# Kernel tuning notes

Measured on AMD Instinct MI355X. Metric: run time of the kernel, lower is better.

The kernel has to match this reference:

```python
import jax, jax.numpy as jnp
import numpy as np

N = 100000   # node_num
D = 256      # enforce_dim
L = 3        # num_layer
E = 200000   # interactions in update batch
B = 50000    # query pairs
W_DECAY = 1e-06
P = 2 * L + 2          # stacked projections per pair
F = P * P              # pair_wise_feature_dim = 64


def setup_inputs() -> dict:
    key = jax.random.key(0)
    ks = jax.random.split(key, 12)
    std = 1.0 / np.sqrt(D)
    inp = {}
    # random projection tables (layer 0 is the random base; layers 1..L are accumulated state)
    inp['rp0'] = jax.random.normal(ks[0], (N, D), jnp.float32) * std
    inp['rp1'] = jax.random.normal(ks[1], (N, D), jnp.float32) * std
    inp['rp2'] = jax.random.normal(ks[2], (N, D), jnp.float32) * std
    inp['rp3'] = jax.random.normal(ks[3], (N, D), jnp.float32) * std
    # sorted interaction timestamps in [0, 1e6]; next_time = times[-1]
    inp['times'] = jnp.sort(jax.random.uniform(ks[4], (E,), jnp.float32) * 1e6)
    inp['now_time'] = jnp.zeros((1,), jnp.float32)
    # MLP: 64 -> 256 -> 64 (stored as [in, out])
    inp['w1'] = jax.random.normal(ks[5], (F, 4 * F), jnp.float32) * (1.0 / np.sqrt(F))
    inp['b1'] = jnp.zeros((4 * F,), jnp.float32)
    inp['w2'] = jax.random.normal(ks[6], (4 * F, F), jnp.float32) * (1.0 / np.sqrt(4 * F))
    inp['b2'] = jnp.zeros((F,), jnp.float32)
    inp['src_ids'] = jax.random.randint(ks[7], (E,), 0, N, jnp.int32)
    inp['dst_ids'] = jax.random.randint(ks[8], (E,), 0, N, jnp.int32)
    inp['q_src'] = jax.random.randint(ks[9], (B,), 0, N, jnp.int32)
    inp['q_dst'] = jax.random.randint(ks[10], (B,), 0, N, jnp.int32)
    return inp


def _update_and_pairwise(rp0, rp1, rp2, rp3, times, now_time, w1, b1, w2, b2,
                         src_ids, dst_ids, q_src, q_dst):
    next_time = times[-1]
    decay = jnp.exp(-W_DECAY * (next_time - now_time[0]))
    # decay accumulated tables: rp[i] *= decay**i for i >= 1
    rps = [rp0, rp1 * decay, rp2 * decay ** 2, rp3 * decay ** 3]
    tw = jnp.exp(-W_DECAY * (next_time - times))[:, None]   # [E,1]
    # update(): for each layer i (all using the pre-update rp[i-1]):
    #   rp[i][src] += rp[i-1][dst] * tw ; rp[i][dst] += rp[i-1][src] * tw
    new = [rps[0]]
    for i in range(1, L + 1):
        upd = rps[i].at[src_ids].add(rps[i - 1][dst_ids] * tw)
        upd = upd.at[dst_ids].add(rps[i - 1][src_ids] * tw)
        new.append(upd)
    # get_pair_wise_feature()
    src_proj = jnp.stack([r[q_src] for r in new], axis=1)   # [B, L+1, D]
    dst_proj = jnp.stack([r[q_dst] for r in new], axis=1)   # [B, L+1, D]
    proj = jnp.concatenate([src_proj, dst_proj], axis=1)    # [B, P, D]
    gram = jnp.einsum('bpd,bqd->bpq', proj, proj).reshape(proj.shape[0], -1)  # [B, F]
    feat = jnp.log1p(jnp.maximum(gram, 0.0))                # not_scale=False path
    h = jax.nn.relu(feat @ w1 + b1)
    return h @ w2 + b2                                      # [B, F]


def reference(rp0, rp1, rp2, rp3, times, now_time, w1, b1, w2, b2,
              src_ids, dst_ids, q_src, q_dst):
    return _update_and_pairwise(rp0, rp1, rp2, rp3, times, now_time,
                                w1, b1, w2, b2, src_ids, dst_ids, q_src, q_dst)
```

## Files before the change

### kernel.cpp

```cpp
#include <hip/hip_runtime.h>
#include <math.h>

#define D 256
#define WDECAY 1e-6f
#define CHUNK 1024
#define MLP_P 64
#define P1 32
#define P2 32


__global__ __launch_bounds__(256) void hist_kernel(
    const int* __restrict__ src, const int* __restrict__ dst, int E,
    int* __restrict__ cnt)
{
    int i = blockIdx.x * blockDim.x + threadIdx.x;
    if (i < 2 * E) {
        int n = (i < E) ? src[i] : dst[i - E];
        atomicAdd(&cnt[n], 1);
    }
}

__global__ __launch_bounds__(256) void scan_partial(
    const int* __restrict__ cnt, int N, int* __restrict__ bsum)
{
    __shared__ int sdata[256];
    int b = blockIdx.x, t = threadIdx.x;
    int base = b * CHUNK + 4 * t;
    int s = 0;
    if (base + 3 < N) {
        int4 v = *(const int4*)(cnt + base);
        s = v.x + v.y + v.z + v.w;
    } else {
        for (int k = 0; k < 4; ++k)
            if (base + k < N) s += cnt[base + k];
    }
    sdata[t] = s;
    __syncthreads();
    for (int off = 128; off > 0; off >>= 1) {
        if (t < off) sdata[t] += sdata[t + off];
        __syncthreads();
    }
    if (t == 0) bsum[b] = sdata[0];
}

__global__ __launch_bounds__(256) void scan_blocksums(
    int* __restrict__ bsum, int NB, int* __restrict__ row_start, int N)
{
    __shared__ int part[256];
    int t = threadIdx.x;
    int per = (NB + 255) / 256;
    int lo = t * per, hi = lo + per;
    if (hi > NB) hi = NB;
    int s = 0;
    for (int i = lo; i < hi; ++i) s += bsum[i];
    part[t] = s;
    __syncthreads();
    for (int off = 1; off < 256; off <<= 1) {
        int v = (t >= off) ? part[t - off] : 0;
        __syncthreads();
        part[t] += v;
        __syncthreads();
    }
    int base = (t == 0) ? 0 : part[t - 1];
    for (int i = lo; i < hi; ++i) {
        int c = bsum[i];
        bsum[i] = base;
        base += c;
    }
    if (t == 255) row_start[N] = part[255];
}

__global__ __launch_bounds__(256) void scan_apply(
    int* __restrict__ cnt, const int* __restrict__ bsum,
    int* __restrict__ row_start, int N)
{
    __shared__ int part[256];
    int b = blockIdx.x, t = threadIdx.x;
    int base = b * CHUNK + 4 * t;
    int4 v = make_int4(0, 0, 0, 0);
    if (base + 3 < N) {
        v = *(const int4*)(cnt + base);
    } else {
        if (base + 0 < N) v.x = cnt[base + 0];
        if (base + 1 < N) v.y = cnt[base + 1];
        if (base + 2 < N) v.z = cnt[base + 2];
    }
    part[t] = v.x + v.y + v.z + v.w;
    __syncthreads();
    for (int off = 1; off < 256; off <<= 1) {
        int pv = (t >= off) ? part[t - off] : 0;
        __syncthreads();
        part[t] += pv;
        __syncthreads();
    }
    int p = bsum[b] + ((t == 0) ? 0 : part[t - 1]);
    int p0 = p, p1 = p0 + v.x, p2 = p1 + v.y, p3 = p2 + v.z;
    if (base + 0 < N) { row_start[base + 0] = p0; cnt[base + 0] = p0; }
    if (base + 1 < N) { row_start[base + 1] = p1; cnt[base + 1] = p1; }
    if (base + 2 < N) { row_start[base + 2] = p2; cnt[base + 2] = p2; }
    if (base + 3 < N) { row_start[base + 3] = p3; cnt[base + 3] = p3; }
}

__global__ __launch_bounds__(256) void fill_kernel(
    const int* __restrict__ src, const int* __restrict__ dst,
    const float* __restrict__ times, int E,
    int* __restrict__ cursor, int* __restrict__ adj_other,
    float* __restrict__ adj_tw)
{
    int i = blockIdx.x * blockDim.x + threadIdx.x;
    if (i >= 2 * E) return;
    int e = (i < E) ? i : i - E;
    int node  = (i < E) ? src[e] : dst[e];
    int other = (i < E) ? dst[e] : src[e];
    float tlast = times[E - 1];
    float w = expf(-WDECAY * (tlast - times[e]));
    int pos = atomicAdd(&cursor[node], 1);
    adj_other[pos] = other;
    adj_tw[pos] = w;
}

__global__ __launch_bounds__(256) void set_flags(
    const int* __restrict__ qs, const int* __restrict__ qd, int B,
    int* __restrict__ flag)
{
    int i = blockIdx.x * blockDim.x + threadIdx.x;
    if (i < B) {
        flag[qs[i]] = 1;
        flag[qd[i]] = 1;
    }
}

__global__ __launch_bounds__(64) void apply_updates(
    const float* __restrict__ rp0, const float* __restrict__ rp1,
    const float* __restrict__ rp2, const float* __restrict__ rp3,
    const float* __restrict__ times, const float* __restrict__ now_time, int E,
    const int* __restrict__ row_start, const int* __restrict__ adj_other,
    const float* __restrict__ adj_tw, const int* __restrict__ flag,
    float* __restrict__ new1, float* __restrict__ new2, float* __restrict__ new3)
{
    int n = blockIdx.x;
    if (!flag[n]) return;
    int l = blockIdx.y;
    int lid = threadIdx.x;
    float tlast = times[E - 1];
    float dec = expf(-WDECAY * (tlast - now_time[0]));

    const float* own; const float* gat; float* outp; float os, gs;
    if (l == 0)      { own = rp1; gat = rp0; outp = new1; os = dec;             gs = 1.f;       }
    else if (l == 1) { own = rp2; gat = rp1; outp = new2; os = dec * dec;       gs = dec;       }
    else             { own = rp3; gat = rp2; outp = new3; os = dec * dec * dec; gs = dec * dec; }

    long long base = (long long)n * D + lid * 4;
    float4 acc = *(const float4*)(own + base);
    acc.x *= os; acc.y *= os; acc.z *= os; acc.w *= os;

    int s = row_start[n];
    int e = row_start[n + 1];
    for (int j = s; j < e; ++j) {
        int o = adj_other[j];
        float w = adj_tw[j] * gs;
        float4 v = *(const float4*)(gat + (long long)o * D + lid * 4);
        acc.x += v.x * w; acc.y += v.y * w; acc.z += v.z * w; acc.w += v.w * w;
    }
    *(float4*)(outp + base) = acc;
}


__global__ __launch_bounds__(64) void gather_gram(
    const float* __restrict__ rp0, const float* __restrict__ new1,
    const float* __restrict__ new2, const float* __restrict__ new3,
    const int* __restrict__ q_src, const int* __restrict__ q_dst,
    float* __restrict__ feat, int B)
{
    __shared__ float proj[8][260];
    int b = blockIdx.x;
    int lid = threadIdx.x;
    long long qs = q_src[b];
    long long qd = q_dst[b];

    const float* tabs[4] = {rp0, new1, new2, new3};
    #pragma unroll
    for (int r = 0; r < 4; ++r) {
        const float* tp = tabs[r];
        float4 v = *(const float4*)(tp + qs * D + lid * 4);
        *(float4*)&proj[r][lid * 4] = v;
        float4 w = *(const float4*)(tp + qd * D + lid * 4);
        *(float4*)&proj[r + 4][lid * 4] = w;
    }
    __syncthreads();

    int p = lid >> 3;
    int q = lid & 7;
    float acc = 0.f;
    #pragma unroll 8
    for (int k = 0; k < 64; ++k) {
        float4 a = *(const float4*)&proj[p][4 * k];
        float4 c = *(const float4*)&proj[q][4 * k];
        acc += a.x * c.x + a.y * c.y + a.z * c.z + a.w * c.w;
    }
    feat[(long long)b * 64 + lid] = log1pf(fmaxf(acc, 0.f));
}

__global__ __launch_bounds__(256, 2) void mlp1_kernel(
    const float* __restrict__ feat,
    const float* __restrict__ w1,
    const float* __restrict__ b1,
    float* __restrict__ H,
    int B)
{
    __shared__ float w1s[64][256];
    __shared__ float fsT[64][36];
    int t = threadIdx.x;
    int p0 = blockIdx.x * P1;

    {
        const float4* wg = (const float4*)w1;
        float4* wd = (float4*)&w1s[0][0];
        #pragma unroll
        for (int r = 0; r < 16; ++r) wd[t + 256 * r] = wg[t + 256 * r];
    }
    #pragma unroll
    for (int r = 0; r < 8; ++r) {
        int idx = t + 256 * r;
        int p = idx >> 6;
        int k = idx & 63;
        int gp = p0 + p;
        fsT[k][p] = (gp < B) ? feat[(long long)gp * 64 + k] : 0.f;
    }
    __syncthreads();

    int tp = t >> 6;
    int to = t & 63;
    float4 acc[8];
    #pragma unroll
    for (int i = 0; i < 8; ++i) acc[i] = make_float4(0.f, 0.f, 0.f, 0.f);

    #pragma unroll 4
    for (int k = 0; k < 64; ++k) {
        float4 fA = *(const float4*)&fsT[k][tp * 8];
        float4 fB = *(const float4*)&fsT[k][tp * 8 + 4];
        float4 wv = *(const float4*)&w1s[k][to * 4];
        float f_[8] = {fA.x, fA.y, fA.z, fA.w, fB.x, fB.y, fB.z, fB.w};
        #pragma unroll
        for (int i = 0; i < 8; ++i) {
            acc[i].x += f_[i] * wv.x; acc[i].y += f_[i] * wv.y;
            acc[i].z += f_[i] * wv.z; acc[i].w += f_[i] * wv.w;
        }
    }

    float4 bv = *(const float4*)&b1[to * 4];
    #pragma unroll
    for (int i = 0; i < 8; ++i) {
        int gp = p0 + tp * 8 + i;
        if (gp < B) {
            float4 h = make_float4(fmaxf(acc[i].x + bv.x, 0.f),
                                   fmaxf(acc[i].y + bv.y, 0.f),
                                   fmaxf(acc[i].z + bv.z, 0.f),
                                   fmaxf(acc[i].w + bv.w, 0.f));
            *(float4*)&H[(long long)gp * 256 + to * 4] = h;
        }
    }
}

__global__ __launch_bounds__(256, 2) void mlp2_kernel(
    const float* __restrict__ H,
    const float* __restrict__ w2,
    const float* __restrict__ b2,
    float* __restrict__ out, int B)
{
    __shared__ float Hs[P2][260];
    int t = threadIdx.x;
    int p0 = blockIdx.x * P2;

    #pragma unroll
    for (int r = 0; r < 8; ++r) {
        int idx = t + 256 * r;
        int p = idx >> 6;
        int k4 = idx & 63;
        int gp = p0 + p;
        float4 v = (gp < B) ? *(const float4*)&H[(long long)gp * 256 + k4 * 4]
                            : make_float4(0.f, 0.f, 0.f, 0.f);
        *(float4*)&Hs[p][k4 * 4] = v;
    }
    __syncthreads();

    int tp2 = t >> 4;
    int tc  = t & 15;
    float4 a0 = make_float4(0.f, 0.f, 0.f, 0.f);
    float4 a1 = make_float4(0.f, 0.f, 0.f, 0.f);

    #pragma unroll 2
    for (int k = 0; k < 256; k += 4) {
        float4 h0 = *(const float4*)&Hs[tp2 * 2 + 0][k];
        float4 h1 = *(const float4*)&Hs[tp2 * 2 + 1][k];
        float4 w0 = *(const float4*)&w2[(k + 0) * 64 + tc * 4];
        float4 w1v = *(const float4*)&w2[(k + 1) * 64 + tc * 4];
        float4 w2v = *(const float4*)&w2[(k + 2) * 64 + tc * 4];
        float4 w3 = *(const float4*)&w2[(k + 3) * 64 + tc * 4];
        a0.x += h0.x * w0.x + h0.y * w1v.x + h0.z * w2v.x + h0.w * w3.x;
        a0.y += h0.x * w0.y + h0.y * w1v.y + h0.z * w2v.y + h0.w * w3.y;
        a0.z += h0.x * w0.z + h0.y * w1v.z + h0.z * w2v.z + h0.w * w3.z;
        a0.w += h0.x * w0.w + h0.y * w1v.w + h0.z * w2v.w + h0.w * w3.w;
        a1.x += h1.x * w0.x + h1.y * w1v.x + h1.z * w2v.x + h1.w * w3.x;
        a1.y += h1.x * w0.y + h1.y * w1v.y + h1.z * w2v.y + h1.w * w3.y;
        a1.z += h1.x * w0.z + h1.y * w1v.z + h1.z * w2v.z + h1.w * w3.z;
        a1.w += h1.x * w0.w + h1.y * w1v.w + h1.z * w2v.w + h1.w * w3.w;
    }

    float4 bv = *(const float4*)&b2[tc * 4];
    int gp0 = p0 + tp2 * 2;
    if (gp0 < B)
        *(float4*)&out[(long long)gp0 * 64 + tc * 4] =
            make_float4(a0.x + bv.x, a0.y + bv.y, a0.z + bv.z, a0.w + bv.w);
    if (gp0 + 1 < B)
        *(float4*)&out[(long long)(gp0 + 1) * 64 + tc * 4] =
            make_float4(a1.x + bv.x, a1.y + bv.y, a1.z + bv.z, a1.w + bv.w);
}

__global__ __launch_bounds__(256, 1) void mlp_fused(
    const float* __restrict__ feat,
    const float* __restrict__ w1,
    const float* __restrict__ b1,
    const float* __restrict__ w2,
    const float* __restrict__ b2,
    float* __restrict__ out, int B)
{
    __shared__ float fsT[64][68];
    __shared__ float w1s[64 * 256];
    __shared__ float hT[256][65];
    int t = threadIdx.x;
    int p0 = blockIdx.x * MLP_P;

    {
        const float4* wg = (const float4*)w1;
        float4* wd = (float4*)w1s;
        #pragma unroll
        for (int r = 0; r < 16; ++r) wd[t + 256 * r] = wg[t + 256 * r];
    }
    #pragma unroll
    for (int r = 0; r < 16; ++r) {
        int idx = t + 256 * r;
        int p = idx >> 6;
        int k = idx & 63;
        int gp = p0 + p;
        fsT[k][p] = (gp < B) ? feat[(long long)gp * 64 + k] : 0.f;
    }
    __syncthreads();

    {
        int tp = t >> 5;
        int to = t & 31;
        float acc[8][8];
        #pragma unroll
        for (int i = 0; i < 8; ++i)
            #pragma unroll
            for (int j = 0; j < 8; ++j) acc[i][j] = 0.f;

        #pragma unroll 4
        for (int k = 0; k < 64; ++k) {
            float4 fA = *(const float4*)&fsT[k][tp * 8];
            float4 fB = *(const float4*)&fsT[k][tp * 8 + 4];
            const float* wr = w1s + k * 256 + to;
            float w[8];
            #pragma unroll
            for (int j = 0; j < 8; ++j) w[j] = wr[32 * j];
            float f0 = fA.x, f1 = fA.y, f2 = fA.z, f3 = fA.w;
            float f4 = fB.x, f5 = fB.y, f6 = fB.z, f7 = fB.w;
            #pragma unroll
            for (int j = 0; j < 8; ++j) {
                acc[0][j] += f0 * w[j]; acc[1][j] += f1 * w[j];
                acc[2][j] += f2 * w[j]; acc[3][j] += f3 * w[j];
                acc[4][j] += f4 * w[j]; acc[5][j] += f5 * w[j];
                acc[6][j] += f6 * w[j]; acc[7][j] += f7 * w[j];
            }
        }
        #pragma unroll
        for (int j = 0; j < 8; ++j) {
            int o = to + 32 * j;
            float bb = b1[o];
            #pragma unroll
            for (int i = 0; i < 8; ++i)
                hT[o][tp * 8 + i] = fmaxf(acc[i][j] + bb, 0.f);
        }
    }
    __syncthreads();

    {
        int tp2 = t >> 4;
        int tc  = t & 15;
        float a0x = 0.f, a0y = 0.f, a0z = 0.f, a0w = 0.f;
        float a1x = 0.f, a1y = 0.f, a1z = 0.f, a1w = 0.f;
        float a2x = 0.f, a2y = 0.f, a2z = 0.f, a2w = 0.f;
        float a3x = 0.f, a3y = 0.f, a3z = 0.f, a3w = 0.f;

        #pragma unroll 8
        for (int k = 0; k < 256; ++k) {
            float h0 = hT[k][tp2 * 4 + 0];
            float h1 = hT[k][tp2 * 4 + 1];
            float h2 = hT[k][tp2 * 4 + 2];
            float h3 = hT[k][tp2 * 4 + 3];
            float4 wv = *(const float4*)&w2[k * 64 + tc * 4];
            a0x += h0 * wv.x; a0y += h0 * wv.y; a0z += h0 * wv.z; a0w += h0 * wv.w;
            a1x += h1 * wv.x; a1y += h1 * wv.y; a1z += h1 * wv.z; a1w += h1 * wv.w;
            a2x += h2 * wv.x; a2y += h2 * wv.y; a2z += h2 * wv.z; a2w += h2 * wv.w;
            a3x += h3 * wv.x; a3y += h3 * wv.y; a3z += h3 * wv.z; a3w += h3 * wv.w;
        }
        float4 bv = *(const float4*)&b2[tc * 4];
        int gp = p0 + tp2 * 4;
        float* op = out + (long long)gp * 64 + tc * 4;
        if (gp + 0 < B) *(float4*)(op + 0 * 64) =
            make_float4(a0x + bv.x, a0y + bv.y, a0z + bv.z, a0w + bv.w);
        if (gp + 1 < B) *(float4*)(op + 1 * 64) =
            make_float4(a1x + bv.x, a1y + bv.y, a1z + bv.z, a1w + bv.w);
        if (gp + 2 < B) *(float4*)(op + 2 * 64) =
            make_float4(a2x + bv.x, a2y + bv.y, a2z + bv.z, a2w + bv.w);
        if (gp + 3 < B) *(float4*)(op + 3 * 64) =
            make_float4(a3x + bv.x, a3y + bv.y, a3z + bv.z, a3w + bv.w);
    }
}


__global__ __launch_bounds__(256) void init_tables(
    const float* __restrict__ rp1, const float* __restrict__ rp2,
    const float* __restrict__ rp3, const float* __restrict__ times,
    const float* __restrict__ now_time, int E,
    float* __restrict__ new1, float* __restrict__ new2, float* __restrict__ new3,
    long long n4)
{
    float tlast = times[E - 1];
    float dec = expf(-WDECAY * (tlast - now_time[0]));
    float d2 = dec * dec;
    float d3 = d2 * dec;
    const float4* r1 = (const float4*)rp1;
    const float4* r2 = (const float4*)rp2;
    const float4* r3 = (const float4*)rp3;
    float4* n1 = (float4*)new1;
    float4* n2 = (float4*)new2;
    float4* n3 = (float4*)new3;
    long long i = (long long)blockIdx.x * blockDim.x + threadIdx.x;
    long long stride = (long long)gridDim.x * blockDim.x;
    for (; i < n4; i += stride) {
        float4 a = r1[i]; a.x *= dec; a.y *= dec; a.z *= dec; a.w *= dec; n1[i] = a;
        float4 b = r2[i]; b.x *= d2; b.y *= d2; b.z *= d2; b.w *= d2; n2[i] = b;
        float4 c = r3[i]; c.x *= d3; c.y *= d3; c.z *= d3; c.w *= d3; n3[i] = c;
    }
}

__global__ __launch_bounds__(256) void scatter_edges(
    const float* __restrict__ rp0, const float* __restrict__ rp1,
    const float* __restrict__ rp2, const float* __restrict__ times,
    const float* __restrict__ now_time,
    const int* __restrict__ src_ids, const int* __restrict__ dst_ids, int E,
    float* __restrict__ new1, float* __restrict__ new2, float* __restrict__ new3)
{
    int e = blockIdx.x;
    int d = threadIdx.x;
    float tlast = times[E - 1];
    float dec = expf(-WDECAY * (tlast - now_time[0]));
    float d2 = dec * dec;
    float tw = expf(-WDECAY * (tlast - times[e]));
    long long s = src_ids[e];
    long long t = dst_ids[e];
    long long so = s * D + d;
    long long to = t * D + d;
    float a0s = rp0[so], a0t = rp0[to];
    atomicAdd(&new1[so], a0t * tw);
    atomicAdd(&new1[to], a0s * tw);
    float a1s = rp1[so] * dec, a1t = rp1[to] * dec;
    atomicAdd(&new2[so], a1t * tw);
    atomicAdd(&new2[to], a1s * tw);
    float a2s = rp2[so] * d2, a2t = rp2[to] * d2;
    atomicAdd(&new3[so], a2t * tw);
    atomicAdd(&new3[to], a2s * tw);
}

__global__ __launch_bounds__(64) void pair_feature_mlp(
    const float* __restrict__ rp0, const float* __restrict__ new1,
    const float* __restrict__ new2, const float* __restrict__ new3,
    const int* __restrict__ q_src, const int* __restrict__ q_dst,
    const float* __restrict__ w1, const float* __restrict__ b1,
    const float* __restrict__ w2, const float* __restrict__ b2,
    float* __restrict__ out, int B)
{
    __shared__ float proj[8][260];
    __shared__ float feat_s[64];
    __shared__ float h_s[256];

    int b = blockIdx.x;
    int lid = threadIdx.x;
    long long qs = q_src[b];
    long long qd = q_dst[b];

    const float* tabs[4] = {rp0, new1, new2, new3};
    #pragma unroll
    for (int r = 0; r < 4; ++r) {
        const float* tp = tabs[r];
        float4 v = *(const float4*)(tp + qs * D + lid * 4);
        *(float4*)&proj[r][lid * 4] = v;
        float4 w = *(const float4*)(tp + qd * D + lid * 4);
        *(float4*)&proj[r + 4][lid * 4] = w;
    }
    __syncthreads();

    int p = lid >> 3;
    int q = lid & 7;
    float acc = 0.f;
    #pragma unroll 8
    for (int k = 0; k < 64; ++k) {
        float4 a = *(const float4*)&proj[p][4 * k];
        float4 c = *(const float4*)&proj[q][4 * k];
        acc += a.x * c.x + a.y * c.y + a.z * c.z + a.w * c.w;
    }
    feat_s[lid] = log1pf(fmaxf(acc, 0.f));
    __syncthreads();

    float4 hv = *(const float4*)(b1 + 4 * lid);
    #pragma unroll 4
    for (int i = 0; i < 64; ++i) {
        float fv = feat_s[i];
        float4 w = *(const float4*)(w1 + i * 256 + 4 * lid);
        hv.x += fv * w.x; hv.y += fv * w.y; hv.z += fv * w.z; hv.w += fv * w.w;
    }
    *(float4*)&h_s[4 * lid] = make_float4(fmaxf(hv.x, 0.f), fmaxf(hv.y, 0.f),
                                          fmaxf(hv.z, 0.f), fmaxf(hv.w, 0.f));
    __syncthreads();

    float o0 = 0.f, o1 = 0.f, o2 = 0.f, o3 = 0.f;
    #pragma unroll 4
    for (int j = 0; j < 256; j += 4) {
        o0 += h_s[j + 0] * w2[(j + 0) * 64 + lid];
        o1 += h_s[j + 1] * w2[(j + 1) * 64 + lid];
        o2 += h_s[j + 2] * w2[(j + 2) * 64 + lid];
        o3 += h_s[j + 3] * w2[(j + 3) * 64 + lid];
    }
    out[(long long)b * 64 + lid] = b2[lid] + (o0 + o1) + (o2 + o3);
}

extern "C" void kernel_launch(void* const* d_in, const int* in_sizes, int n_in,
                              void* d_out, int out_size, void* d_ws, size_t ws_size,
                              hipStream_t stream)
{
    const float* rp0      = (const float*)d_in[0];
    const float* rp1      = (const float*)d_in[1];
    const float* rp2      = (const float*)d_in[2];
    const float* rp3      = (const float*)d_in[3];
    const float* times    = (const float*)d_in[4];
    const float* now_time = (const float*)d_in[5];
    const float* w1       = (const float*)d_in[6];
    const float* b1       = (const float*)d_in[7];
    const float* w2       = (const float*)d_in[8];
    const float* b2       = (const float*)d_in[9];
    const int*   src_ids  = (const int*)d_in[10];
    const int*   dst_ids  = (const int*)d_in[11];
    const int*   q_src    = (const int*)d_in[12];
    const int*   q_dst    = (const int*)d_in[13];
    float* out = (float*)d_out;

    long long ND = in_sizes[0];
    int N = (int)(ND / D);
    int E = in_sizes[4];
    int B = in_sizes[12];
    int NB = (N + CHUNK - 1) / CHUNK;

    float* new1 = (float*)d_ws;
    float* new2 = new1 + ND;
    float* new3 = new2 + ND;

    size_t base_bytes = (size_t)3 * ND * sizeof(float);
    size_t csr_bytes  = (size_t)(2 * N + (N + 1) + 2 * E + NB) * sizeof(int)
                      + (size_t)(2 * E) * sizeof(float)
                      + (size_t)B * 64 * sizeof(float);
    size_t h_bytes    = (size_t)B * 256 * sizeof(float);

    if (ws_size >= base_bytes + csr_bytes && NB <= 65536) {
        int* cnt       = (int*)(new3 + ND);
        int* flag      = cnt + N;
        int* row_start = flag + N;
        int* adj_other = row_start + N + 1;
        float* adj_tw  = (float*)(adj_other + 2 * E);
        int* bsum      = (int*)(adj_tw + 2 * E);
        float* feat    = (float*)(bsum + NB);
        float* Hbuf    = feat + (size_t)B * 64;
        bool   split   = (ws_size >= base_bytes + csr_bytes + h_bytes);

        hipMemsetAsync(cnt, 0, (size_t)2 * N * sizeof(int), stream);
        int twoE = 2 * E;
        hist_kernel<<<(twoE + 255) / 256, 256, 0, stream>>>(src_ids, dst_ids, E, cnt);
        set_flags<<<(B + 255) / 256, 256, 0, stream>>>(q_src, q_dst, B, flag);
        scan_partial<<<NB, 256, 0, stream>>>(cnt, N, bsum);
        scan_blocksums<<<1, 256, 0, stream>>>(bsum, NB, row_start, N);
        scan_apply<<<NB, 256, 0, stream>>>(cnt, bsum, row_start, N);
        fill_kernel<<<(twoE + 255) / 256, 256, 0, stream>>>(src_ids, dst_ids, times, E,
                                                            cnt, adj_other, adj_tw);
        dim3 grid(N, 3);
        apply_updates<<<grid, 64, 0, stream>>>(rp0, rp1, rp2, rp3, times, now_time, E,
                                               row_start, adj_other, adj_tw, flag,
                                               new1, new2, new3);
        gather_gram<<<B, 64, 0, stream>>>(rp0, new1, new2, new3, q_src, q_dst, feat, B);
        if (split) {
            mlp1_kernel<<<(B + P1 - 1) / P1, 256, 0, stream>>>(feat, w1, b1, Hbuf, B);
            mlp2_kernel<<<(B + P2 - 1) / P2, 256, 0, stream>>>(Hbuf, w2, b2, out, B);
        } else {
            mlp_fused<<<(B + MLP_P - 1) / MLP_P, 256, 0, stream>>>(feat, w1, b1, w2, b2,
                                                                   out, B);
        }
    } else {
        long long n4 = ND / 4;
        init_tables<<<2048, 256, 0, stream>>>(rp1, rp2, rp3, times, now_time, E,
                                              new1, new2, new3, n4);
        scatter_edges<<<E, 256, 0, stream>>>(rp0, rp1, rp2, times, now_time,
                                             src_ids, dst_ids, E, new1, new2, new3);
        pair_feature_mlp<<<B, 64, 0, stream>>>(rp0, new1, new2, new3, q_src, q_dst,
                                               w1, b1, w2, b2, out, B);
    }
}
```

Baseline: 643.4 us.

## Compute gram in registers with butterfly shuffle reduction, four pairs per block

```diff
diff --git a/kernel.cpp b/kernel.cpp
--- a/kernel.cpp
+++ b/kernel.cpp
@@ -166,39 +166,91 @@
 }
 
 
-__global__ __launch_bounds__(64) void gather_gram(
+__global__ __launch_bounds__(256) void gather_gram(
     const float* __restrict__ rp0, const float* __restrict__ new1,
     const float* __restrict__ new2, const float* __restrict__ new3,
     const int* __restrict__ q_src, const int* __restrict__ q_dst,
     float* __restrict__ feat, int B)
 {
-    __shared__ float proj[8][260];
-    int b = blockIdx.x;
-    int lid = threadIdx.x;
+    int b = blockIdx.x * 4 + (threadIdx.x >> 6);
+    int lid = threadIdx.x & 63;
+    if (b >= B) return;
     long long qs = q_src[b];
     long long qd = q_dst[b];
 
     const float* tabs[4] = {rp0, new1, new2, new3};
+    float4 v[8];
     #pragma unroll
     for (int r = 0; r < 4; ++r) {
-        const float* tp = tabs[r];
-        float4 v = *(const float4*)(tp + qs * D + lid * 4);
-        *(float4*)&proj[r][lid * 4] = v;
-        float4 w = *(const float4*)(tp + qd * D + lid * 4);
-        *(float4*)&proj[r + 4][lid * 4] = w;
-    }
-    __syncthreads();
-
-    int p = lid >> 3;
-    int q = lid & 7;
-    float acc = 0.f;
-    #pragma unroll 8
-    for (int k = 0; k < 64; ++k) {
-        float4 a = *(const float4*)&proj[p][4 * k];
-        float4 c = *(const float4*)&proj[q][4 * k];
-        acc += a.x * c.x + a.y * c.y + a.z * c.z + a.w * c.w;
-    }
-    feat[(long long)b * 64 + lid] = log1pf(fmaxf(acc, 0.f));
+        v[r]     = *(const float4*)(tabs[r] + qs * D + lid * 4);
+        v[r + 4] = *(const float4*)(tabs[r] + qd * D + lid * 4);
+    }
+
+    float red[64];
+    #pragma unroll
+    for (int p = 0; p < 8; ++p) {
+        #pragma unroll
+        for (int q = p; q < 8; ++q) {
+            float d = v[p].x * v[q].x + v[p].y * v[q].y
+                    + v[p].z * v[q].z + v[p].w * v[q].w;
+            red[p * 8 + q] = d;
+            red[q * 8 + p] = d;
+        }
+    }
+
+    {
+        bool hi = (lid & 32) != 0;
+        #pragma unroll
+        for (int i = 0; i < 32; ++i) {
+            float send = hi ? red[i] : red[i + 32];
+            float keep = hi ? red[i + 32] : red[i];
+            red[i] = keep + __shfl_xor(send, 32, 64);
+        }
+    }
+    {
+        bool hi = (lid & 16) != 0;
+        #pragma unroll
+        for (int i = 0; i < 16; ++i) {
+            float send = hi ? red[i] : red[i + 16];
+            float keep = hi ? red[i + 16] : red[i];
+            red[i] = keep + __shfl_xor(send, 16, 64);
+        }
+    }
+    {
+        bool hi = (lid & 8) != 0;
+        #pragma unroll
+        for (int i = 0; i < 8; ++i) {
+            float send = hi ? red[i] : red[i + 8];
+            float keep = hi ? red[i + 8] : red[i];
+            red[i] = keep + __shfl_xor(send, 8, 64);
+        }
+    }
+    {
+        bool hi = (lid & 4) != 0;
+        #pragma unroll
+        for (int i = 0; i < 4; ++i) {
+            float send = hi ? red[i] : red[i + 4];
+            float keep = hi ? red[i + 4] : red[i];
+            red[i] = keep + __shfl_xor(send, 4, 64);
+        }
+    }
+    {
+        bool hi = (lid & 2) != 0;
+        #pragma unroll
+        for (int i = 0; i < 2; ++i) {
+            float send = hi ? red[i] : red[i + 2];
+            float keep = hi ? red[i + 2] : red[i];
+            red[i] = keep + __shfl_xor(send, 2, 64);
+        }
+    }
+    {
+        bool hi = (lid & 1) != 0;
+        float send = hi ? red[0] : red[1];
+        float keep = hi ? red[1] : red[0];
+        red[0] = keep + __shfl_xor(send, 1, 64);
+    }
+
+    feat[(long long)b * 64 + lid] = log1pf(fmaxf(red[0], 0.f));
 }
 
 __global__ __launch_bounds__(256, 2) void mlp1_kernel(
@@ -596,7 +648,8 @@
         apply_updates<<<grid, 64, 0, stream>>>(rp0, rp1, rp2, rp3, times, now_time, E,
                                                row_start, adj_other, adj_tw, flag,
                                                new1, new2, new3);
-        gather_gram<<<B, 64, 0, stream>>>(rp0, new1, new2, new3, q_src, q_dst, feat, B);
+        gather_gram<<<(B + 3) / 4, 256, 0, stream>>>(rp0, new1, new2, new3,
+                                                     q_src, q_dst, feat, B);
         if (split) {
             mlp1_kernel<<<(B + P1 - 1) / P1, 256, 0, stream>>>(feat, w1, b1, Hbuf, B);
             mlp2_kernel<<<(B + P2 - 1) / P2, 256, 0, stream>>>(Hbuf, w2, b2, out, B);
```

Measured after the change: 641.2 us. No clear change (-0.3%).
